# Kernel tuning notes

Hardware: AMD Instinct MI355X
Metric: run time of the kernel (lower is better)

## Reference

```python
import jax, jax.numpy as jnp
import numpy as np

TEMPERATURE = 0.5
IRRELEVANCE_THRESHOLD = 0.4
LN_EPS = 1e-5
NORM_EPS = 1e-12


def setup_inputs() -> dict:
    key = jax.random.key(0)
    ks = jax.random.split(key, 8)
    B, T, D = 32, 4096, 256  # D = 4 * config.embed_dim
    H = D // 2  # relevance encoder output dim = 128
    x = jax.random.normal(ks[0], (B, T, D), dtype=jnp.float32)
    W1 = jax.random.normal(ks[1], (D, D), dtype=jnp.float32) * (1.0 / np.sqrt(D))
    b1 = jnp.zeros((D,), dtype=jnp.float32)
    ln_g = jnp.ones((D,), dtype=jnp.float32)
    ln_b = jnp.zeros((D,), dtype=jnp.float32)
    W2 = jax.random.normal(ks[2], (D, H), dtype=jnp.float32) * (1.0 / np.sqrt(D))
    b2 = jnp.zeros((H,), dtype=jnp.float32)
    topic_query = jax.random.normal(ks[3], (1, 1, D), dtype=jnp.float32)
    spectral_filter = jnp.ones((4,), dtype=jnp.float32) * 0.5
    return {"x": x, "W1": W1, "b1": b1, "ln_g": ln_g, "ln_b": ln_b,
            "W2": W2, "b2": b2, "topic_query": topic_query,
            "spectral_filter": spectral_filter}


def _encode(h, W1, b1, ln_g, ln_b, W2, b2):
    # Linear -> LayerNorm -> GELU(exact) -> Linear
    h = h @ W1 + b1
    mu = jnp.mean(h, axis=-1, keepdims=True)
    var = jnp.mean((h - mu) ** 2, axis=-1, keepdims=True)
    h = (h - mu) / jnp.sqrt(var + LN_EPS) * ln_g + ln_b
    h = jax.nn.gelu(h, approximate=False)
    return h @ W2 + b2


def _l2norm(v):
    n = jnp.sqrt(jnp.sum(v * v, axis=-1, keepdims=True))
    return v / jnp.maximum(n, NORM_EPS)


def reference(x, W1, b1, ln_g, ln_b, W2, b2, topic_query, spectral_filter):
    B, T, D = x.shape
    # --- extract main topic: learned-query attention over time ---
    q = jnp.broadcast_to(topic_query, (B, 1, D))
    scores = jnp.einsum('bqd,btd->bqt', q, x) / TEMPERATURE  # [B,1,T]
    weights = jax.nn.softmax(scores, axis=-1)
    main_topic = jnp.einsum('bqt,btd->bqd', weights, x)  # [B,1,D]
    # --- relevance scores: cosine sim in encoded space ---
    x_enc = _encode(x, W1, b1, ln_g, ln_b, W2, b2)            # [B,T,D/2]
    t_enc = _encode(main_topic, W1, b1, ln_g, ln_b, W2, b2)   # [B,1,D/2]
    relevance = jnp.sum(_l2norm(x_enc) * _l2norm(t_enc), axis=-1)  # [B,T]
    # --- masked complex spectral filtering on quaternion view ---
    irrelevant = relevance < IRRELEVANCE_THRESHOLD  # [B,T]
    x_quat = x.reshape(B, T, D // 4, 4)
    x_fft = jnp.fft.fft(x_quat, axis=1)  # complex64 [B,T,D/4,4]
    filt = jnp.exp(1j * spectral_filter.astype(jnp.complex64))  # [4]
    x_fft = jnp.where(irrelevant[:, :, None, None], x_fft * filt, x_fft)
    x_filtered = jnp.fft.ifft(x_fft, axis=1).real
    return x_filtered.reshape(B, T, D)
```

## Files before the change

kernel.cpp:

```cpp
#include <hip/hip_runtime.h>
#include <math.h>

typedef float f32x4 __attribute__((ext_vector_type(4)));
typedef __bf16 bh8 __attribute__((ext_vector_type(8)));

constexpr int Bc = 32;
constexpr int Tc = 4096;
constexpr int Dc = 256;
constexpr int Hc = 128;
constexpr float kTempInv = 2.0f;
constexpr float kThr = 0.4f;
constexpr float kLnEps = 1e-5f;
constexpr float kNormEps = 1e-12f;
constexpr float kInvSqrt2 = 0.70710678118654752440f;

__device__ __forceinline__ unsigned short f2bf(float f) {
  unsigned u = __float_as_uint(f);
  u += 0x7FFFu + ((u >> 16) & 1u);
  return (unsigned short)(u >> 16);
}
__device__ __forceinline__ float bf2f(unsigned short s) {
  return __uint_as_float(((unsigned)s) << 16);
}

__global__ __launch_bounds__(256) void k_scores(const float* __restrict__ x,
                                                const float* __restrict__ tq,
                                                float* __restrict__ scores) {
  const int wave = threadIdx.x >> 6;
  const int lane = threadIdx.x & 63;
  const int base = blockIdx.x * 32 + wave * 8;
  const float4 q4 = reinterpret_cast<const float4*>(tq)[lane];
  for (int i = 0; i < 8; ++i) {
    const int tok = base + i;
    const float4 xv = reinterpret_cast<const float4*>(x + (size_t)tok * Dc)[lane];
    float p = xv.x * q4.x + xv.y * q4.y + xv.z * q4.z + xv.w * q4.w;
    #pragma unroll
    for (int off = 32; off > 0; off >>= 1) p += __shfl_xor(p, off, 64);
    if (lane == 0) scores[tok] = p * kTempInv;
  }
}

__global__ __launch_bounds__(1024) void k_smstats(const float* __restrict__ scores,
                                                  float2* __restrict__ stats) {
  const int b = blockIdx.x, tid = threadIdx.x;
  const float4 v = reinterpret_cast<const float4*>(scores + (size_t)b * Tc)[tid];
  __shared__ float red[16];
  float m = fmaxf(fmaxf(v.x, v.y), fmaxf(v.z, v.w));
  #pragma unroll
  for (int off = 32; off > 0; off >>= 1) m = fmaxf(m, __shfl_xor(m, off, 64));
  if ((tid & 63) == 0) red[tid >> 6] = m;
  __syncthreads();
  if (tid == 0) {
    float gm = red[0];
    for (int i = 1; i < 16; ++i) gm = fmaxf(gm, red[i]);
    red[0] = gm;
  }
  __syncthreads();
  const float gmax = red[0];
  float s = expf(v.x - gmax) + expf(v.y - gmax) + expf(v.z - gmax) + expf(v.w - gmax);
  #pragma unroll
  for (int off = 32; off > 0; off >>= 1) s += __shfl_xor(s, off, 64);
  __syncthreads();
  if ((tid & 63) == 0) red[tid >> 6] = s;
  __syncthreads();
  if (tid == 0) {
    float t = 0.0f;
    for (int i = 0; i < 16; ++i) t += red[i];
    stats[b] = make_float2(gmax, t);
  }
}

__global__ __launch_bounds__(256) void k_wsum(const float* __restrict__ x,
                                              const float* __restrict__ scores,
                                              const float2* __restrict__ stats,
                                              float* __restrict__ mt) {
  const int b = blockIdx.x >> 4;
  const int chunk = blockIdx.x & 15;
  const int d = threadIdx.x;
  const float2 st = stats[b];
  const int t0 = chunk * 256;
  const float* xb = x + ((size_t)b * Tc + t0) * Dc + d;
  const float* sb = scores + (size_t)b * Tc + t0;
  float acc = 0.0f;
  for (int i = 0; i < 256; ++i) {
    const float w = expf(sb[i] - st.x);
    acc += w * xb[(size_t)i * Dc];
  }
  atomicAdd(&mt[b * Dc + d], acc * (1.0f / st.y));
}

__global__ __launch_bounds__(256) void k_tenc(
    const float* __restrict__ mt, const float* __restrict__ W1,
    const float* __restrict__ b1, const float* __restrict__ lng,
    const float* __restrict__ lnb, const float* __restrict__ W2,
    const float* __restrict__ b2, float* __restrict__ tnorm) {
  const int b = blockIdx.x, j = threadIdx.x;
  __shared__ float v[Dc];
  __shared__ float g[Dc];
  __shared__ float red[4];
  v[j] = mt[b * Dc + j];
  __syncthreads();
  float h = b1[j];
  for (int k = 0; k < Dc; ++k) h += v[k] * W1[(size_t)k * Dc + j];
  float s = h;
  #pragma unroll
  for (int off = 32; off > 0; off >>= 1) s += __shfl_xor(s, off, 64);
  if ((j & 63) == 0) red[j >> 6] = s;
  __syncthreads();
  const float mu = (red[0] + red[1] + red[2] + red[3]) * (1.0f / Dc);
  __syncthreads();
  const float dev = h - mu;
  float q = dev * dev;
  #pragma unroll
  for (int off = 32; off > 0; off >>= 1) q += __shfl_xor(q, off, 64);
  if ((j & 63) == 0) red[j >> 6] = q;
  __syncthreads();
  const float var = (red[0] + red[1] + red[2] + red[3]) * (1.0f / Dc);
  float hn = dev / sqrtf(var + kLnEps) * lng[j] + lnb[j];
  hn = 0.5f * hn * (1.0f + erff(hn * kInvSqrt2));
  g[j] = hn;
  __syncthreads();
  float z = 0.0f;
  if (j < Hc) {
    z = b2[j];
    for (int k = 0; k < Dc; ++k) z += g[k] * W2[(size_t)k * Hc + j];
  }
  float q2 = z * z;
  #pragma unroll
  for (int off = 32; off > 0; off >>= 1) q2 += __shfl_xor(q2, off, 64);
  __syncthreads();
  if ((j & 63) == 0) red[j >> 6] = q2;
  __syncthreads();
  if (j < Hc) {
    const float nrm = sqrtf(red[0] + red[1] + red[2] + red[3]);
    tnorm[b * Hc + j] = z / fmaxf(nrm, kNormEps);
  }
}

__global__ __launch_bounds__(256) void k_prep(const float* __restrict__ W1,
                                              const float* __restrict__ W2,
                                              unsigned short* __restrict__ w1h,
                                              unsigned short* __restrict__ w1l,
                                              unsigned short* __restrict__ w2h,
                                              unsigned short* __restrict__ w2l) {
  const int g = blockIdx.x * 256 + threadIdx.x;
  if (blockIdx.x < 64) {
    const int n = g >> 6;
    const int kq = (g & 63) * 4;
    unsigned h[2] = {0, 0}, l[2] = {0, 0};
    #pragma unroll
    for (int j = 0; j < 4; ++j) {
      const float v = W1[(size_t)(kq + j) * Dc + n];
      const unsigned short hb = f2bf(v);
      const unsigned short lb = f2bf(v - bf2f(hb));
      h[j >> 1] |= ((unsigned)hb) << ((j & 1) * 16);
      l[j >> 1] |= ((unsigned)lb) << ((j & 1) * 16);
    }
    *reinterpret_cast<uint2*>(&w1h[(size_t)n * Dc + kq]) = make_uint2(h[0], h[1]);
    *reinterpret_cast<uint2*>(&w1l[(size_t)n * Dc + kq]) = make_uint2(l[0], l[1]);
  } else {
    const int g2 = g - 16384;
    const int n = g2 >> 6;
    const int kq = (g2 & 63) * 4;
    unsigned h[2] = {0, 0}, l[2] = {0, 0};
    #pragma unroll
    for (int j = 0; j < 4; ++j) {
      const float v = W2[(size_t)(kq + j) * Hc + n];
      const unsigned short hb = f2bf(v);
      const unsigned short lb = f2bf(v - bf2f(hb));
      h[j >> 1] |= ((unsigned)hb) << ((j & 1) * 16);
      l[j >> 1] |= ((unsigned)lb) << ((j & 1) * 16);
    }
    *reinterpret_cast<uint2*>(&w2h[(size_t)n * Dc + kq]) = make_uint2(h[0], h[1]);
    *reinterpret_cast<uint2*>(&w2l[(size_t)n * Dc + kq]) = make_uint2(l[0], l[1]);
  }
}

__global__ __launch_bounds__(256, 2) void k_encode_mfma(
    const float* __restrict__ x,
    const unsigned short* __restrict__ w1h, const unsigned short* __restrict__ w1l,
    const unsigned short* __restrict__ w2h, const unsigned short* __restrict__ w2l,
    const float* __restrict__ b1, const float* __restrict__ lng,
    const float* __restrict__ lnb, const float* __restrict__ b2,
    const float* __restrict__ tnorm, unsigned char* __restrict__ irr) {
  constexpr int LDB = 264;
  constexpr int LDH = 260;
  __shared__ __align__(16) char uni[64 * LDB * 2 * 2];
  __shared__ float ps[2][64];
  __shared__ float psD[2][64];
  __shared__ float p_b1[Dc], p_g[Dc], p_bb[Dc], p_b2[Hc], p_tn[Hc];
  unsigned short* xh_hi = reinterpret_cast<unsigned short*>(uni);
  unsigned short* xh_lo = xh_hi + 64 * LDB;
  float* hbuf = reinterpret_cast<float*>(uni);

  const int tid = threadIdx.x;
  const size_t tok0 = (size_t)blockIdx.x * 64;
  const int b = (int)(tok0 >> 12);
  const int lane = tid & 63;
  const int wave = tid >> 6;
  const int wm = wave >> 1, wn = wave & 1;
  const int lrow = lane & 15, lkh = lane >> 4;

  p_b1[tid] = b1[tid];
  p_g[tid] = lng[tid];
  p_bb[tid] = lnb[tid];
  if (tid < Hc) {
    p_b2[tid] = b2[tid];
    p_tn[tid] = tnorm[b * Hc + tid];
  }
  #pragma unroll
  for (int i = 0; i < 16; ++i) {
    const int f = tid + (i << 8);
    const int row = f >> 6, c4 = f & 63;
    const float4 v = reinterpret_cast<const float4*>(x + (tok0 + row) * Dc)[c4];
    unsigned hp[2] = {0, 0}, lp[2] = {0, 0};
    const float vv[4] = {v.x, v.y, v.z, v.w};
    #pragma unroll
    for (int j = 0; j < 4; ++j) {
      const unsigned short hb = f2bf(vv[j]);
      const unsigned short lb = f2bf(vv[j] - bf2f(hb));
      hp[j >> 1] |= ((unsigned)hb) << ((j & 1) * 16);
      lp[j >> 1] |= ((unsigned)lb) << ((j & 1) * 16);
    }
    *reinterpret_cast<uint2*>(&xh_hi[row * LDB + c4 * 4]) = make_uint2(hp[0], hp[1]);
    *reinterpret_cast<uint2*>(&xh_lo[row * LDB + c4 * 4]) = make_uint2(lp[0], lp[1]);
  }
  __syncthreads();

  f32x4 acc1[2][8];
  #pragma unroll
  for (int mt = 0; mt < 2; ++mt)
    #pragma unroll
    for (int nt = 0; nt < 8; ++nt) acc1[mt][nt] = (f32x4){0.f, 0.f, 0.f, 0.f};

  for (int ks = 0; ks < 8; ++ks) {
    bh8 ah[2], al[2];
    #pragma unroll
    for (int mt = 0; mt < 2; ++mt) {
      const int off = (wm * 32 + mt * 16 + lrow) * LDB + ks * 32 + lkh * 8;
      ah[mt] = *reinterpret_cast<const bh8*>(&xh_hi[off]);
      al[mt] = *reinterpret_cast<const bh8*>(&xh_lo[off]);
    }
    #pragma unroll
    for (int nt = 0; nt < 8; ++nt) {
      const size_t boff = (size_t)(wn * 128 + nt * 16 + lrow) * Dc + ks * 32 + lkh * 8;
      const bh8 bh = *reinterpret_cast<const bh8*>(&w1h[boff]);
      const bh8 bl = *reinterpret_cast<const bh8*>(&w1l[boff]);
      #pragma unroll
      for (int mt = 0; mt < 2; ++mt) {
        acc1[mt][nt] = __builtin_amdgcn_mfma_f32_16x16x32_bf16(ah[mt], bh, acc1[mt][nt], 0, 0, 0);
        acc1[mt][nt] = __builtin_amdgcn_mfma_f32_16x16x32_bf16(al[mt], bh, acc1[mt][nt], 0, 0, 0);
        acc1[mt][nt] = __builtin_amdgcn_mfma_f32_16x16x32_bf16(ah[mt], bl, acc1[mt][nt], 0, 0, 0);
      }
    }
  }
  __syncthreads();

  float s[2][4];
  #pragma unroll
  for (int mt = 0; mt < 2; ++mt)
    #pragma unroll
    for (int j = 0; j < 4; ++j) s[mt][j] = 0.0f;
  #pragma unroll
  for (int nt = 0; nt < 8; ++nt) {
    const int col = wn * 128 + nt * 16 + lrow;
    const float bv = p_b1[col];
    #pragma unroll
    for (int mt = 0; mt < 2; ++mt) {
      #pragma unroll
      for (int j = 0; j < 4; ++j) {
        acc1[mt][nt][j] += bv;
        s[mt][j] += acc1[mt][nt][j];
      }
    }
  }
  #pragma unroll
  for (int mt = 0; mt < 2; ++mt)
    #pragma unroll
    for (int j = 0; j < 4; ++j) {
      #pragma unroll
      for (int off = 8; off > 0; off >>= 1) s[mt][j] += __shfl_xor(s[mt][j], off, 64);
    }
  if (lrow == 0) {
    #pragma unroll
    for (int mt = 0; mt < 2; ++mt)
      #pragma unroll
      for (int j = 0; j < 4; ++j)
        ps[wn][wm * 32 + mt * 16 + lkh * 4 + j] = s[mt][j];
  }
  __syncthreads();
  float mu[2][4];
  #pragma unroll
  for (int mt = 0; mt < 2; ++mt)
    #pragma unroll
    for (int j = 0; j < 4; ++j) {
      const int r = wm * 32 + mt * 16 + lkh * 4 + j;
      mu[mt][j] = (ps[0][r] + ps[1][r]) * (1.0f / Dc);
    }
  float q[2][4];
  #pragma unroll
  for (int mt = 0; mt < 2; ++mt)
    #pragma unroll
    for (int j = 0; j < 4; ++j) q[mt][j] = 0.0f;
  #pragma unroll
  for (int nt = 0; nt < 8; ++nt)
    #pragma unroll
    for (int mt = 0; mt < 2; ++mt)
      #pragma unroll
      for (int j = 0; j < 4; ++j) {
        const float d = acc1[mt][nt][j] - mu[mt][j];
        q[mt][j] += d * d;
      }
  #pragma unroll
  for (int mt = 0; mt < 2; ++mt)
    #pragma unroll
    for (int j = 0; j < 4; ++j) {
      #pragma unroll
      for (int off = 8; off > 0; off >>= 1) q[mt][j] += __shfl_xor(q[mt][j], off, 64);
    }
  if (lrow == 0) {
    #pragma unroll
    for (int mt = 0; mt < 2; ++mt)
      #pragma unroll
      for (int j = 0; j < 4; ++j)
        psD[wn][wm * 32 + mt * 16 + lkh * 4 + j] = q[mt][j];
  }
  __syncthreads();
  float inv[2][4];
  #pragma unroll
  for (int mt = 0; mt < 2; ++mt)
    #pragma unroll
    for (int j = 0; j < 4; ++j) {
      const int r = wm * 32 + mt * 16 + lkh * 4 + j;
      const float var = (psD[0][r] + psD[1][r]) * (1.0f / Dc);
      inv[mt][j] = 1.0f / sqrtf(var + kLnEps);
    }
  #pragma unroll
  for (int nt = 0; nt < 8; ++nt) {
    const int col = wn * 128 + nt * 16 + lrow;
    const float gv = p_g[col], bb = p_bb[col];
    #pragma unroll
    for (int mt = 0; mt < 2; ++mt)
      #pragma unroll
      for (int j = 0; j < 4; ++j) {
        float hv = (acc1[mt][nt][j] - mu[mt][j]) * inv[mt][j] * gv + bb;
        hv = 0.5f * hv * (1.0f + erff(hv * kInvSqrt2));
        hbuf[(wm * 32 + mt * 16 + lkh * 4 + j) * LDH + col] = hv;
      }
  }
  __syncthreads();

  f32x4 acc2[2][4];
  #pragma unroll
  for (int mt = 0; mt < 2; ++mt)
    #pragma unroll
    for (int nt = 0; nt < 4; ++nt) acc2[mt][nt] = (f32x4){0.f, 0.f, 0.f, 0.f};

  for (int ks = 0; ks < 8; ++ks) {
    bh8 ah[2], al[2];
    #pragma unroll
    for (int mt = 0; mt < 2; ++mt) {
      const int base = (wm * 32 + mt * 16 + lrow) * LDH + ks * 32 + lkh * 8;
      const f32x4 u0 = *reinterpret_cast<const f32x4*>(&hbuf[base]);
      const f32x4 u1 = *reinterpret_cast<const f32x4*>(&hbuf[base + 4]);
      union { unsigned short us[8]; bh8 v; } uh, ul;
      #pragma unroll
      for (int j = 0; j < 4; ++j) {
        const unsigned short hb = f2bf(u0[j]);
        uh.us[j] = hb;
        ul.us[j] = f2bf(u0[j] - bf2f(hb));
      }
      #pragma unroll
      for (int j = 0; j < 4; ++j) {
        const unsigned short hb = f2bf(u1[j]);
        uh.us[4 + j] = hb;
        ul.us[4 + j] = f2bf(u1[j] - bf2f(hb));
      }
      ah[mt] = uh.v;
      al[mt] = ul.v;
    }
    #pragma unroll
    for (int nt = 0; nt < 4; ++nt) {
      const size_t boff = (size_t)(wn * 64 + nt * 16 + lrow) * Dc + ks * 32 + lkh * 8;
      const bh8 bh = *reinterpret_cast<const bh8*>(&w2h[boff]);
      const bh8 bl = *reinterpret_cast<const bh8*>(&w2l[boff]);
      #pragma unroll
      for (int mt = 0; mt < 2; ++mt) {
        acc2[mt][nt] = __builtin_amdgcn_mfma_f32_16x16x32_bf16(ah[mt], bh, acc2[mt][nt], 0, 0, 0);
        acc2[mt][nt] = __builtin_amdgcn_mfma_f32_16x16x32_bf16(al[mt], bh, acc2[mt][nt], 0, 0, 0);
        acc2[mt][nt] = __builtin_amdgcn_mfma_f32_16x16x32_bf16(ah[mt], bl, acc2[mt][nt], 0, 0, 0);
      }
    }
  }

  float ss[2][4], sd[2][4];
  #pragma unroll
  for (int mt = 0; mt < 2; ++mt)
    #pragma unroll
    for (int j = 0; j < 4; ++j) { ss[mt][j] = 0.0f; sd[mt][j] = 0.0f; }
  #pragma unroll
  for (int nt = 0; nt < 4; ++nt) {
    const int col2 = wn * 64 + nt * 16 + lrow;
    const float b2v = p_b2[col2], tv = p_tn[col2];
    #pragma unroll
    for (int mt = 0; mt < 2; ++mt)
      #pragma unroll
      for (int j = 0; j < 4; ++j) {
        const float z = acc2[mt][nt][j] + b2v;
        ss[mt][j] += z * z;
        sd[mt][j] += z * tv;
      }
  }
  #pragma unroll
  for (int mt = 0; mt < 2; ++mt)
    #pragma unroll
    for (int j = 0; j < 4; ++j) {
      #pragma unroll
      for (int off = 8; off > 0; off >>= 1) {
        ss[mt][j] += __shfl_xor(ss[mt][j], off, 64);
        sd[mt][j] += __shfl_xor(sd[mt][j], off, 64);
      }
    }
  if (lrow == 0) {
    #pragma unroll
    for (int mt = 0; mt < 2; ++mt)
      #pragma unroll
      for (int j = 0; j < 4; ++j) {
        const int r = wm * 32 + mt * 16 + lkh * 4 + j;
        ps[wn][r] = ss[mt][j];
        psD[wn][r] = sd[mt][j];
      }
  }
  __syncthreads();
  if (tid < 64) {
    const float S = ps[0][tid] + ps[1][tid];
    const float Dd = psD[0][tid] + psD[1][tid];
    const float rel = Dd / fmaxf(sqrtf(S), kNormEps);
    irr[tok0 + tid] = (rel < kThr) ? (unsigned char)1 : (unsigned char)0;
  }
}

__global__ __launch_bounds__(256) void k_transpose(const float* __restrict__ in,
                                                   float* __restrict__ out,
                                                   int R, int C) {
  __shared__ float t[64][65];
  const int tilesC = C >> 6;
  const int perB = (R >> 6) * tilesC;
  const int bid = blockIdx.x;
  const int b = bid / perB;
  const int rem = bid % perB;
  const int tr = rem / tilesC, tc = rem % tilesC;
  const float* ib = in + (size_t)b * R * C;
  float* ob = out + (size_t)b * R * C;
  const int c = threadIdx.x & 63;
  const int r0 = threadIdx.x >> 6;
  #pragma unroll
  for (int i = 0; i < 16; ++i) {
    const int r = r0 + i * 4;
    t[r][c] = ib[(size_t)(tr * 64 + r) * C + tc * 64 + c];
  }
  __syncthreads();
  #pragma unroll
  for (int i = 0; i < 16; ++i) {
    const int r = r0 + i * 4;
    ob[(size_t)(tc * 64 + r) * R + tr * 64 + c] = t[c][r];
  }
}

__device__ __forceinline__ void fft_stages(float2* bufA, float2* bufB,
                                           const float2* tw, int tid, float sign) {
  float2* src = bufA;
  float2* dst = bufB;
  int s = 1;
  for (int stage = 0; stage < 12; ++stage) {
    const int notm = ~(s - 1);
    #pragma unroll
    for (int i = 0; i < 8; ++i) {
      const int r = tid + (i << 8);
      const float2 a = src[r];
      const float2 b = src[r + 2048];
      const float2 w = tw[r & notm];
      const float wy = w.y * sign;
      const float dr = a.x - b.x;
      const float di = a.y - b.y;
      const int d0 = r + (r & notm);
      dst[d0] = make_float2(a.x + b.x, a.y + b.y);
      dst[d0 + s] = make_float2(dr * w.x - di * wy, dr * wy + di * w.x);
    }
    __syncthreads();
    float2* t = src; src = dst; dst = t;
    s <<= 1;
  }
}

__device__ __forceinline__ void mask_pair(float2* buf, const unsigned char* __restrict__ irb,
                                          int k, float ca, float sa, float cb, float sb) {
  const int m = (4096 - k) & 4095;
  const bool ik = irb[k] != 0;
  const bool im = irb[m] != 0;
  const float2 Zk = buf[k];
  const float2 Zm = buf[m];
  const float Ar = 0.5f * (Zk.x + Zm.x), Ai = 0.5f * (Zk.y - Zm.y);
  const float Br = 0.5f * (Zk.y + Zm.y), Bi = -0.5f * (Zk.x - Zm.x);
  const float Gar = 0.5f * ((ik ? ca : 1.0f) + (im ? ca : 1.0f));
  const float Gai = 0.5f * ((ik ? sa : 0.0f) - (im ? sa : 0.0f));
  const float Gbr = 0.5f * ((ik ? cb : 1.0f) + (im ? cb : 1.0f));
  const float Gbi = 0.5f * ((ik ? sb : 0.0f) - (im ? sb : 0.0f));
  const float har = Gar * Ar - Gai * Ai, hai = Gar * Ai + Gai * Ar;
  const float hbr = Gbr * Br - Gbi * Bi, hbi = Gbr * Bi + Gbi * Br;
  buf[k] = make_float2(har - hbi, hai + hbr);
  buf[m] = make_float2(har + hbi, hbr - hai);
}

__global__ __launch_bounds__(256) void k_fft_filter(const float* __restrict__ x,
                                                    const unsigned char* __restrict__ irr,
                                                    const float* __restrict__ sf,
                                                    float* __restrict__ out) {
  __shared__ float2 bufA[4096];
  __shared__ float2 bufB[4096];
  __shared__ float2 tw[2048];
  const int b = blockIdx.x >> 7;
  const int pr = blockIdx.x & 127;
  const int c0 = pr * 2;
  const int tid = threadIdx.x;
  for (int i = tid; i < 2048; i += 256) {
    float sn, cn;
    sincosf(-1.5339807878856412e-3f * (float)i, &sn, &cn);
    tw[i] = make_float2(cn, sn);
  }
  const float* xb = x + ((size_t)b * Tc) * Dc + c0;
  #pragma unroll
  for (int i = 0; i < 16; ++i) {
    const int t = tid + (i << 8);
    bufA[t] = *reinterpret_cast<const float2*>(xb + (size_t)t * Dc);
  }
  __syncthreads();
  fft_stages(bufA, bufB, tw, tid, 1.0f);
  float sa, ca, sb, cb;
  sincosf(sf[c0 & 3], &sa, &ca);
  sincosf(sf[(c0 + 1) & 3], &sb, &cb);
  const unsigned char* irb = irr + (size_t)b * Tc;
  #pragma unroll
  for (int i = 0; i < 8; ++i) mask_pair(bufA, irb, tid + (i << 8), ca, sa, cb, sb);
  if (tid == 0) mask_pair(bufA, irb, 2048, ca, sa, cb, sb);
  __syncthreads();
  fft_stages(bufA, bufB, tw, tid, -1.0f);
  float* ob = out + ((size_t)b * Tc) * Dc + c0;
  constexpr float invN = 1.0f / 4096.0f;
  #pragma unroll
  for (int i = 0; i < 16; ++i) {
    const int t = tid + (i << 8);
    const float2 y = bufA[t];
    *reinterpret_cast<float2*>(ob + (size_t)t * Dc) = make_float2(y.x * invN, y.y * invN);
  }
}

__global__ __launch_bounds__(256) void k_fft_filterT(float* __restrict__ xT,
                                                     const unsigned char* __restrict__ irr,
                                                     const float* __restrict__ sf) {
  __shared__ float2 bufA[4096];
  __shared__ float2 bufB[4096];
  __shared__ float2 tw[2048];
  const int b = blockIdx.x >> 7;
  const int pr = blockIdx.x & 127;
  const int c0 = pr * 2;
  const int tid = threadIdx.x;
  for (int i = tid; i < 2048; i += 256) {
    float sn, cn;
    sincosf(-1.5339807878856412e-3f * (float)i, &sn, &cn);
    tw[i] = make_float2(cn, sn);
  }
  float* r0 = xT + (size_t)(b * Dc + c0) * Tc;
  float* r1 = r0 + Tc;
  #pragma unroll
  for (int i = 0; i < 4; ++i) {
    const int idx = tid + (i << 8);
    const float4 a0 = reinterpret_cast<const float4*>(r0)[idx];
    const float4 a1 = reinterpret_cast<const float4*>(r1)[idx];
    const int t4 = idx * 4;
    bufA[t4 + 0] = make_float2(a0.x, a1.x);
    bufA[t4 + 1] = make_float2(a0.y, a1.y);
    bufA[t4 + 2] = make_float2(a0.z, a1.z);
    bufA[t4 + 3] = make_float2(a0.w, a1.w);
  }
  __syncthreads();
  fft_stages(bufA, bufB, tw, tid, 1.0f);
  float sa, ca, sb, cb;
  sincosf(sf[c0 & 3], &sa, &ca);
  sincosf(sf[(c0 + 1) & 3], &sb, &cb);
  const unsigned char* irb = irr + (size_t)b * Tc;
  #pragma unroll
  for (int i = 0; i < 8; ++i) mask_pair(bufA, irb, tid + (i << 8), ca, sa, cb, sb);
  if (tid == 0) mask_pair(bufA, irb, 2048, ca, sa, cb, sb);
  __syncthreads();
  fft_stages(bufA, bufB, tw, tid, -1.0f);
  constexpr float invN = 1.0f / 4096.0f;
  #pragma unroll
  for (int i = 0; i < 4; ++i) {
    const int idx = tid + (i << 8);
    const int t4 = idx * 4;
    const float2 y0 = bufA[t4 + 0], y1 = bufA[t4 + 1];
    const float2 y2 = bufA[t4 + 2], y3 = bufA[t4 + 3];
    reinterpret_cast<float4*>(r0)[idx] =
        make_float4(y0.x * invN, y1.x * invN, y2.x * invN, y3.x * invN);
    reinterpret_cast<float4*>(r1)[idx] =
        make_float4(y0.y * invN, y1.y * invN, y2.y * invN, y3.y * invN);
  }
}

extern "C" void kernel_launch(void* const* d_in, const int* in_sizes, int n_in,
                              void* d_out, int out_size, void* d_ws, size_t ws_size,
                              hipStream_t stream) {
  const float* x   = (const float*)d_in[0];
  const float* W1  = (const float*)d_in[1];
  const float* b1  = (const float*)d_in[2];
  const float* lng = (const float*)d_in[3];
  const float* lnb = (const float*)d_in[4];
  const float* W2  = (const float*)d_in[5];
  const float* b2  = (const float*)d_in[6];
  const float* tq  = (const float*)d_in[7];
  const float* sf  = (const float*)d_in[8];
  float* out = (float*)d_out;

  char* ws = (char*)d_ws;
  float* scores        = (float*)(ws);
  unsigned short* w1h  = (unsigned short*)(ws);
  unsigned short* w1l  = (unsigned short*)(ws + 131072);
  unsigned short* w2h  = (unsigned short*)(ws + 262144);
  unsigned short* w2l  = (unsigned short*)(ws + 327680);
  float* mt            = (float*)(ws + 524288);
  float2* stats        = (float2*)(ws + 557056);
  float* tnorm         = (float*)(ws + 557312);
  unsigned char* irr   = (unsigned char*)(ws + 573696);
  float* xT            = (float*)(ws + 2097152);
  const bool bigws = ws_size >= (size_t)2097152 + (size_t)134217728;

  hipMemsetAsync(mt, 0, Bc * Dc * sizeof(float), stream);

  k_scores<<<Bc * Tc / 32, 256, 0, stream>>>(x, tq, scores);
  k_smstats<<<Bc, 1024, 0, stream>>>(scores, stats);
  k_wsum<<<Bc * 16, 256, 0, stream>>>(x, scores, stats, mt);
  k_prep<<<96, 256, 0, stream>>>(W1, W2, w1h, w1l, w2h, w2l);
  k_tenc<<<Bc, 256, 0, stream>>>(mt, W1, b1, lng, lnb, W2, b2, tnorm);
  if (bigws) {
    k_transpose<<<Bc * 64 * 4, 256, 0, stream>>>(x, xT, Tc, Dc);
  }
  k_encode_mfma<<<Bc * Tc / 64, 256, 0, stream>>>(x, w1h, w1l, w2h, w2l,
                                                  b1, lng, lnb, b2, tnorm, irr);
  if (bigws) {
    k_fft_filterT<<<Bc * (Dc / 2), 256, 0, stream>>>(xT, irr, sf);
    k_transpose<<<Bc * 4 * 64, 256, 0, stream>>>(xT, out, Dc, Tc);
  } else {
    k_fft_filter<<<Bc * (Dc / 2), 256, 0, stream>>>(x, irr, sf, out);
  }
}
```

Before: 779.5 us.

## Replace transpose+radix-2 FFT with fused radix-4 FFT and shrink encoder LDS

```diff
diff --git a/kernel.cpp b/kernel.cpp
--- a/kernel.cpp
+++ b/kernel.cpp
@@ -176,22 +176,19 @@
   }
 }
 
-__global__ __launch_bounds__(256, 2) void k_encode_mfma(
+__global__ __launch_bounds__(256, 4) void k_encode_mfma(
     const float* __restrict__ x,
     const unsigned short* __restrict__ w1h, const unsigned short* __restrict__ w1l,
     const unsigned short* __restrict__ w2h, const unsigned short* __restrict__ w2l,
     const float* __restrict__ b1, const float* __restrict__ lng,
     const float* __restrict__ lnb, const float* __restrict__ b2,
     const float* __restrict__ tnorm, unsigned char* __restrict__ irr) {
-  constexpr int LDB = 264;
-  constexpr int LDH = 260;
-  __shared__ __align__(16) char uni[64 * LDB * 2 * 2];
+  constexpr int LH = 136;
+  __shared__ __align__(16) unsigned short s_hi[64 * LH];
+  __shared__ __align__(16) unsigned short s_lo[64 * LH];
   __shared__ float ps[2][64];
   __shared__ float psD[2][64];
   __shared__ float p_b1[Dc], p_g[Dc], p_bb[Dc], p_b2[Hc], p_tn[Hc];
-  unsigned short* xh_hi = reinterpret_cast<unsigned short*>(uni);
-  unsigned short* xh_lo = xh_hi + 64 * LDB;
-  float* hbuf = reinterpret_cast<float*>(uni);
 
   const int tid = threadIdx.x;
   const size_t tok0 = (size_t)blockIdx.x * 64;
@@ -208,24 +205,6 @@
     p_b2[tid] = b2[tid];
     p_tn[tid] = tnorm[b * Hc + tid];
   }
-  #pragma unroll
-  for (int i = 0; i < 16; ++i) {
-    const int f = tid + (i << 8);
-    const int row = f >> 6, c4 = f & 63;
-    const float4 v = reinterpret_cast<const float4*>(x + (tok0 + row) * Dc)[c4];
-    unsigned hp[2] = {0, 0}, lp[2] = {0, 0};
-    const float vv[4] = {v.x, v.y, v.z, v.w};
-    #pragma unroll
-    for (int j = 0; j < 4; ++j) {
-      const unsigned short hb = f2bf(vv[j]);
-      const unsigned short lb = f2bf(vv[j] - bf2f(hb));
-      hp[j >> 1] |= ((unsigned)hb) << ((j & 1) * 16);
-      lp[j >> 1] |= ((unsigned)lb) << ((j & 1) * 16);
-    }
-    *reinterpret_cast<uint2*>(&xh_hi[row * LDB + c4 * 4]) = make_uint2(hp[0], hp[1]);
-    *reinterpret_cast<uint2*>(&xh_lo[row * LDB + c4 * 4]) = make_uint2(lp[0], lp[1]);
-  }
-  __syncthreads();
 
   f32x4 acc1[2][8];
   #pragma unroll
@@ -233,28 +212,59 @@
     #pragma unroll
     for (int nt = 0; nt < 8; ++nt) acc1[mt][nt] = (f32x4){0.f, 0.f, 0.f, 0.f};
 
-  for (int ks = 0; ks < 8; ++ks) {
-    bh8 ah[2], al[2];
-    #pragma unroll
-    for (int mt = 0; mt < 2; ++mt) {
-      const int off = (wm * 32 + mt * 16 + lrow) * LDB + ks * 32 + lkh * 8;
-      ah[mt] = *reinterpret_cast<const bh8*>(&xh_hi[off]);
-      al[mt] = *reinterpret_cast<const bh8*>(&xh_lo[off]);
-    }
-    #pragma unroll
-    for (int nt = 0; nt < 8; ++nt) {
-      const size_t boff = (size_t)(wn * 128 + nt * 16 + lrow) * Dc + ks * 32 + lkh * 8;
-      const bh8 bh = *reinterpret_cast<const bh8*>(&w1h[boff]);
-      const bh8 bl = *reinterpret_cast<const bh8*>(&w1l[boff]);
+  auto stage_half = [&](int kh) {
+    #pragma unroll
+    for (int i = 0; i < 8; ++i) {
+      const int f = tid + (i << 8);
+      const int row = f >> 5, c4 = f & 31;
+      const float4 v = *reinterpret_cast<const float4*>(
+          x + (tok0 + row) * Dc + kh * 128 + c4 * 4);
+      unsigned hp[2] = {0, 0}, lp[2] = {0, 0};
+      const float vv[4] = {v.x, v.y, v.z, v.w};
+      #pragma unroll
+      for (int j = 0; j < 4; ++j) {
+        const unsigned short hb = f2bf(vv[j]);
+        const unsigned short lb = f2bf(vv[j] - bf2f(hb));
+        hp[j >> 1] |= ((unsigned)hb) << ((j & 1) * 16);
+        lp[j >> 1] |= ((unsigned)lb) << ((j & 1) * 16);
+      }
+      *reinterpret_cast<uint2*>(&s_hi[row * LH + c4 * 4]) = make_uint2(hp[0], hp[1]);
+      *reinterpret_cast<uint2*>(&s_lo[row * LH + c4 * 4]) = make_uint2(lp[0], lp[1]);
+    }
+  };
+
+  auto gemm1_half = [&](int kh) {
+    for (int ks = 0; ks < 4; ++ks) {
+      bh8 ah[2], al[2];
       #pragma unroll
       for (int mt = 0; mt < 2; ++mt) {
-        acc1[mt][nt] = __builtin_amdgcn_mfma_f32_16x16x32_bf16(ah[mt], bh, acc1[mt][nt], 0, 0, 0);
-        acc1[mt][nt] = __builtin_amdgcn_mfma_f32_16x16x32_bf16(al[mt], bh, acc1[mt][nt], 0, 0, 0);
-        acc1[mt][nt] = __builtin_amdgcn_mfma_f32_16x16x32_bf16(ah[mt], bl, acc1[mt][nt], 0, 0, 0);
-      }
-    }
-  }
-  __syncthreads();
+        const int off = (wm * 32 + mt * 16 + lrow) * LH + ks * 32 + lkh * 8;
+        ah[mt] = *reinterpret_cast<const bh8*>(&s_hi[off]);
+        al[mt] = *reinterpret_cast<const bh8*>(&s_lo[off]);
+      }
+      #pragma unroll
+      for (int nt = 0; nt < 8; ++nt) {
+        const size_t boff = (size_t)(wn * 128 + nt * 16 + lrow) * Dc +
+                            kh * 128 + ks * 32 + lkh * 8;
+        const bh8 bh = *reinterpret_cast<const bh8*>(&w1h[boff]);
+        const bh8 bl = *reinterpret_cast<const bh8*>(&w1l[boff]);
+        #pragma unroll
+        for (int mt = 0; mt < 2; ++mt) {
+          acc1[mt][nt] = __builtin_amdgcn_mfma_f32_16x16x32_bf16(ah[mt], bh, acc1[mt][nt], 0, 0, 0);
+          acc1[mt][nt] = __builtin_amdgcn_mfma_f32_16x16x32_bf16(al[mt], bh, acc1[mt][nt], 0, 0, 0);
+          acc1[mt][nt] = __builtin_amdgcn_mfma_f32_16x16x32_bf16(ah[mt], bl, acc1[mt][nt], 0, 0, 0);
+        }
+      }
+    }
+  };
+
+  stage_half(0);
+  __syncthreads();
+  gemm1_half(0);
+  __syncthreads();
+  stage_half(1);
+  __syncthreads();
+  gemm1_half(1);
 
   float s[2][4];
   #pragma unroll
@@ -326,29 +336,21 @@
         psD[wn][wm * 32 + mt * 16 + lkh * 4 + j] = q[mt][j];
   }
   __syncthreads();
-  float inv[2][4];
   #pragma unroll
   for (int mt = 0; mt < 2; ++mt)
     #pragma unroll
     for (int j = 0; j < 4; ++j) {
       const int r = wm * 32 + mt * 16 + lkh * 4 + j;
       const float var = (psD[0][r] + psD[1][r]) * (1.0f / Dc);
-      inv[mt][j] = 1.0f / sqrtf(var + kLnEps);
-    }
-  #pragma unroll
-  for (int nt = 0; nt < 8; ++nt) {
-    const int col = wn * 128 + nt * 16 + lrow;
-    const float gv = p_g[col], bb = p_bb[col];
-    #pragma unroll
-    for (int mt = 0; mt < 2; ++mt)
-      #pragma unroll
-      for (int j = 0; j < 4; ++j) {
-        float hv = (acc1[mt][nt][j] - mu[mt][j]) * inv[mt][j] * gv + bb;
+      const float inv = 1.0f / sqrtf(var + kLnEps);
+      #pragma unroll
+      for (int nt = 0; nt < 8; ++nt) {
+        const int col = wn * 128 + nt * 16 + lrow;
+        float hv = (acc1[mt][nt][j] - mu[mt][j]) * inv * p_g[col] + p_bb[col];
         hv = 0.5f * hv * (1.0f + erff(hv * kInvSqrt2));
-        hbuf[(wm * 32 + mt * 16 + lkh * 4 + j) * LDH + col] = hv;
-      }
-  }
-  __syncthreads();
+        acc1[mt][nt][j] = hv;
+      }
+    }
 
   f32x4 acc2[2][4];
   #pragma unroll
@@ -356,42 +358,56 @@
     #pragma unroll
     for (int nt = 0; nt < 4; ++nt) acc2[mt][nt] = (f32x4){0.f, 0.f, 0.f, 0.f};
 
-  for (int ks = 0; ks < 8; ++ks) {
-    bh8 ah[2], al[2];
-    #pragma unroll
-    for (int mt = 0; mt < 2; ++mt) {
-      const int base = (wm * 32 + mt * 16 + lrow) * LDH + ks * 32 + lkh * 8;
-      const f32x4 u0 = *reinterpret_cast<const f32x4*>(&hbuf[base]);
-      const f32x4 u1 = *reinterpret_cast<const f32x4*>(&hbuf[base + 4]);
-      union { unsigned short us[8]; bh8 v; } uh, ul;
-      #pragma unroll
-      for (int j = 0; j < 4; ++j) {
-        const unsigned short hb = f2bf(u0[j]);
-        uh.us[j] = hb;
-        ul.us[j] = f2bf(u0[j] - bf2f(hb));
-      }
-      #pragma unroll
-      for (int j = 0; j < 4; ++j) {
-        const unsigned short hb = f2bf(u1[j]);
-        uh.us[4 + j] = hb;
-        ul.us[4 + j] = f2bf(u1[j] - bf2f(hb));
-      }
-      ah[mt] = uh.v;
-      al[mt] = ul.v;
-    }
-    #pragma unroll
-    for (int nt = 0; nt < 4; ++nt) {
-      const size_t boff = (size_t)(wn * 64 + nt * 16 + lrow) * Dc + ks * 32 + lkh * 8;
-      const bh8 bh = *reinterpret_cast<const bh8*>(&w2h[boff]);
-      const bh8 bl = *reinterpret_cast<const bh8*>(&w2l[boff]);
+  auto hwrite = [&](int half) {
+    if (wn == half) {
+      #pragma unroll
+      for (int nt = 0; nt < 8; ++nt) {
+        const int colg = nt * 16 + lrow;
+        #pragma unroll
+        for (int mt = 0; mt < 2; ++mt)
+          #pragma unroll
+          for (int j = 0; j < 4; ++j) {
+            const int row = wm * 32 + mt * 16 + lkh * 4 + j;
+            const float hv = acc1[mt][nt][j];
+            const unsigned short hb = f2bf(hv);
+            s_hi[row * LH + colg] = hb;
+            s_lo[row * LH + colg] = f2bf(hv - bf2f(hb));
+          }
+      }
+    }
+  };
+  auto gemm2_half = [&](int kh) {
+    for (int ks = 0; ks < 4; ++ks) {
+      bh8 ah[2], al[2];
       #pragma unroll
       for (int mt = 0; mt < 2; ++mt) {
-        acc2[mt][nt] = __builtin_amdgcn_mfma_f32_16x16x32_bf16(ah[mt], bh, acc2[mt][nt], 0, 0, 0);
-        acc2[mt][nt] = __builtin_amdgcn_mfma_f32_16x16x32_bf16(al[mt], bh, acc2[mt][nt], 0, 0, 0);
-        acc2[mt][nt] = __builtin_amdgcn_mfma_f32_16x16x32_bf16(ah[mt], bl, acc2[mt][nt], 0, 0, 0);
-      }
-    }
-  }
+        const int off = (wm * 32 + mt * 16 + lrow) * LH + ks * 32 + lkh * 8;
+        ah[mt] = *reinterpret_cast<const bh8*>(&s_hi[off]);
+        al[mt] = *reinterpret_cast<const bh8*>(&s_lo[off]);
+      }
+      #pragma unroll
+      for (int nt = 0; nt < 4; ++nt) {
+        const size_t boff = (size_t)(wn * 64 + nt * 16 + lrow) * Dc +
+                            kh * 128 + ks * 32 + lkh * 8;
+        const bh8 bh = *reinterpret_cast<const bh8*>(&w2h[boff]);
+        const bh8 bl = *reinterpret_cast<const bh8*>(&w2l[boff]);
+        #pragma unroll
+        for (int mt = 0; mt < 2; ++mt) {
+          acc2[mt][nt] = __builtin_amdgcn_mfma_f32_16x16x32_bf16(ah[mt], bh, acc2[mt][nt], 0, 0, 0);
+          acc2[mt][nt] = __builtin_amdgcn_mfma_f32_16x16x32_bf16(al[mt], bh, acc2[mt][nt], 0, 0, 0);
+          acc2[mt][nt] = __builtin_amdgcn_mfma_f32_16x16x32_bf16(ah[mt], bl, acc2[mt][nt], 0, 0, 0);
+        }
+      }
+    }
+  };
+
+  hwrite(0);
+  __syncthreads();
+  gemm2_half(0);
+  __syncthreads();
+  hwrite(1);
+  __syncthreads();
+  gemm2_half(1);
 
   float ss[2][4], sd[2][4];
   #pragma unroll
@@ -440,56 +456,44 @@
   }
 }
 
-__global__ __launch_bounds__(256) void k_transpose(const float* __restrict__ in,
-                                                   float* __restrict__ out,
-                                                   int R, int C) {
-  __shared__ float t[64][65];
-  const int tilesC = C >> 6;
-  const int perB = (R >> 6) * tilesC;
-  const int bid = blockIdx.x;
-  const int b = bid / perB;
-  const int rem = bid % perB;
-  const int tr = rem / tilesC, tc = rem % tilesC;
-  const float* ib = in + (size_t)b * R * C;
-  float* ob = out + (size_t)b * R * C;
-  const int c = threadIdx.x & 63;
-  const int r0 = threadIdx.x >> 6;
-  #pragma unroll
-  for (int i = 0; i < 16; ++i) {
-    const int r = r0 + i * 4;
-    t[r][c] = ib[(size_t)(tr * 64 + r) * C + tc * 64 + c];
-  }
-  __syncthreads();
-  #pragma unroll
-  for (int i = 0; i < 16; ++i) {
-    const int r = r0 + i * 4;
-    ob[(size_t)(tc * 64 + r) * R + tr * 64 + c] = t[c][r];
-  }
-}
-
-__device__ __forceinline__ void fft_stages(float2* bufA, float2* bufB,
-                                           const float2* tw, int tid, float sign) {
-  float2* src = bufA;
-  float2* dst = bufB;
-  int s = 1;
-  for (int stage = 0; stage < 12; ++stage) {
-    const int notm = ~(s - 1);
-    #pragma unroll
-    for (int i = 0; i < 8; ++i) {
-      const int r = tid + (i << 8);
-      const float2 a = src[r];
-      const float2 b = src[r + 2048];
-      const float2 w = tw[r & notm];
-      const float wy = w.y * sign;
-      const float dr = a.x - b.x;
-      const float di = a.y - b.y;
-      const int d0 = r + (r & notm);
-      dst[d0] = make_float2(a.x + b.x, a.y + b.y);
-      dst[d0 + s] = make_float2(dr * w.x - di * wy, dr * wy + di * w.x);
+__device__ __forceinline__ float2 cmul(const float2 w, const float2 v) {
+  return make_float2(w.x * v.x - w.y * v.y, w.x * v.y + w.y * v.x);
+}
+
+__device__ void fft4_run(float2* A0, float2* B0, float2* A1, float2* B1,
+                         const float2* __restrict__ tw, const int tid,
+                         const float sgn) {
+  float2 *s0 = A0, *d0 = B0, *s1 = A1, *d1 = B1;
+  int sdiv = 1;
+  for (int st = 0; st < 6; ++st) {
+    const int qq = tid & (sdiv - 1);
+    const int ti = tid - qq;
+    float2 w1 = tw[ti];
+    w1.y *= sgn;
+    const float2 w2 = cmul(w1, w1);
+    const float2 w3 = cmul(w2, w1);
+    const int wb = (ti << 2) + qq;
+    #pragma unroll
+    for (int sq = 0; sq < 2; ++sq) {
+      const float2* S = sq ? s1 : s0;
+      float2* D = sq ? d1 : d0;
+      const float2 a = S[tid];
+      const float2 b = S[tid + 1024];
+      const float2 c = S[tid + 2048];
+      const float2 d = S[tid + 3072];
+      const float apcx = a.x + c.x, apcy = a.y + c.y;
+      const float amcx = a.x - c.x, amcy = a.y - c.y;
+      const float bpdx = b.x + d.x, bpdy = b.y + d.y;
+      const float bmdx = (b.x - d.x) * sgn, bmdy = (b.y - d.y) * sgn;
+      D[wb] = make_float2(apcx + bpdx, apcy + bpdy);
+      D[wb + sdiv] = cmul(w1, make_float2(amcx + bmdy, amcy - bmdx));
+      D[wb + 2 * sdiv] = cmul(w2, make_float2(apcx - bpdx, apcy - bpdy));
+      D[wb + 3 * sdiv] = cmul(w3, make_float2(amcx - bmdy, amcy + bmdx));
     }
     __syncthreads();
-    float2* t = src; src = dst; dst = t;
-    s <<= 1;
+    float2* t = s0; s0 = d0; d0 = t;
+    t = s1; s1 = d1; d1 = t;
+    sdiv <<= 2;
   }
 }
 
@@ -512,99 +516,64 @@
   buf[m] = make_float2(har + hbi, hbr - hai);
 }
 
-__global__ __launch_bounds__(256) void k_fft_filter(const float* __restrict__ x,
-                                                    const unsigned char* __restrict__ irr,
-                                                    const float* __restrict__ sf,
-                                                    float* __restrict__ out) {
-  __shared__ float2 bufA[4096];
-  __shared__ float2 bufB[4096];
-  __shared__ float2 tw[2048];
-  const int b = blockIdx.x >> 7;
-  const int pr = blockIdx.x & 127;
-  const int c0 = pr * 2;
+__global__ __launch_bounds__(1024) void k_fft4(const float* __restrict__ x,
+                                               const unsigned char* __restrict__ irr,
+                                               const float* __restrict__ sf,
+                                               float* __restrict__ out) {
+  __shared__ float2 SA0[4096];
+  __shared__ float2 SB0[4096];
+  __shared__ float2 SA1[4096];
+  __shared__ float2 SB1[4096];
+  __shared__ float2 tw[1024];
+  const int bb = blockIdx.x >> 6;
+  const int g = blockIdx.x & 63;
   const int tid = threadIdx.x;
-  for (int i = tid; i < 2048; i += 256) {
+  {
     float sn, cn;
-    sincosf(-1.5339807878856412e-3f * (float)i, &sn, &cn);
-    tw[i] = make_float2(cn, sn);
-  }
-  const float* xb = x + ((size_t)b * Tc) * Dc + c0;
-  #pragma unroll
-  for (int i = 0; i < 16; ++i) {
-    const int t = tid + (i << 8);
-    bufA[t] = *reinterpret_cast<const float2*>(xb + (size_t)t * Dc);
-  }
-  __syncthreads();
-  fft_stages(bufA, bufB, tw, tid, 1.0f);
-  float sa, ca, sb, cb;
-  sincosf(sf[c0 & 3], &sa, &ca);
-  sincosf(sf[(c0 + 1) & 3], &sb, &cb);
-  const unsigned char* irb = irr + (size_t)b * Tc;
-  #pragma unroll
-  for (int i = 0; i < 8; ++i) mask_pair(bufA, irb, tid + (i << 8), ca, sa, cb, sb);
-  if (tid == 0) mask_pair(bufA, irb, 2048, ca, sa, cb, sb);
-  __syncthreads();
-  fft_stages(bufA, bufB, tw, tid, -1.0f);
-  float* ob = out + ((size_t)b * Tc) * Dc + c0;
+    sincosf(-1.5339807878856412e-3f * (float)tid, &sn, &cn);
+    tw[tid] = make_float2(cn, sn);
+  }
+  const float4* xb = reinterpret_cast<const float4*>(x + (size_t)bb * Tc * Dc) + g;
+  #pragma unroll
+  for (int j = 0; j < 4; ++j) {
+    const int t = tid + (j << 10);
+    const float4 v = xb[(size_t)t * 64];
+    SA0[t] = make_float2(v.x, v.y);
+    SA1[t] = make_float2(v.z, v.w);
+  }
+  __syncthreads();
+
+  fft4_run(SA0, SB0, SA1, SB1, tw, tid, 1.0f);
+
+  float ca0, sa0, cb0, sb0, ca1, sa1, cb1, sb1;
+  sincosf(sf[0], &sa0, &ca0);
+  sincosf(sf[1], &sb0, &cb0);
+  sincosf(sf[2], &sa1, &ca1);
+  sincosf(sf[3], &sb1, &cb1);
+  const unsigned char* irb = irr + (size_t)bb * Tc;
+  #pragma unroll
+  for (int i = 0; i < 2; ++i) {
+    const int k = tid + (i << 10);
+    mask_pair(SA0, irb, k, ca0, sa0, cb0, sb0);
+    mask_pair(SA1, irb, k, ca1, sa1, cb1, sb1);
+  }
+  if (tid == 0) {
+    mask_pair(SA0, irb, 2048, ca0, sa0, cb0, sb0);
+    mask_pair(SA1, irb, 2048, ca1, sa1, cb1, sb1);
+  }
+  __syncthreads();
+
+  fft4_run(SA0, SB0, SA1, SB1, tw, tid, -1.0f);
+
+  float4* ob = reinterpret_cast<float4*>(out + (size_t)bb * Tc * Dc) + g;
   constexpr float invN = 1.0f / 4096.0f;
   #pragma unroll
-  for (int i = 0; i < 16; ++i) {
-    const int t = tid + (i << 8);
-    const float2 y = bufA[t];
-    *reinterpret_cast<float2*>(ob + (size_t)t * Dc) = make_float2(y.x * invN, y.y * invN);
-  }
-}
-
-__global__ __launch_bounds__(256) void k_fft_filterT(float* __restrict__ xT,
-                                                     const unsigned char* __restrict__ irr,
-                                                     const float* __restrict__ sf) {
-  __shared__ float2 bufA[4096];
-  __shared__ float2 bufB[4096];
-  __shared__ float2 tw[2048];
-  const int b = blockIdx.x >> 7;
-  const int pr = blockIdx.x & 127;
-  const int c0 = pr * 2;
-  const int tid = threadIdx.x;
-  for (int i = tid; i < 2048; i += 256) {
-    float sn, cn;
-    sincosf(-1.5339807878856412e-3f * (float)i, &sn, &cn);
-    tw[i] = make_float2(cn, sn);
-  }
-  float* r0 = xT + (size_t)(b * Dc + c0) * Tc;
-  float* r1 = r0 + Tc;
-  #pragma unroll
-  for (int i = 0; i < 4; ++i) {
-    const int idx = tid + (i << 8);
-    const float4 a0 = reinterpret_cast<const float4*>(r0)[idx];
-    const float4 a1 = reinterpret_cast<const float4*>(r1)[idx];
-    const int t4 = idx * 4;
-    bufA[t4 + 0] = make_float2(a0.x, a1.x);
-    bufA[t4 + 1] = make_float2(a0.y, a1.y);
-    bufA[t4 + 2] = make_float2(a0.z, a1.z);
-    bufA[t4 + 3] = make_float2(a0.w, a1.w);
-  }
-  __syncthreads();
-  fft_stages(bufA, bufB, tw, tid, 1.0f);
-  float sa, ca, sb, cb;
-  sincosf(sf[c0 & 3], &sa, &ca);
-  sincosf(sf[(c0 + 1) & 3], &sb, &cb);
-  const unsigned char* irb = irr + (size_t)b * Tc;
-  #pragma unroll
-  for (int i = 0; i < 8; ++i) mask_pair(bufA, irb, tid + (i << 8), ca, sa, cb, sb);
-  if (tid == 0) mask_pair(bufA, irb, 2048, ca, sa, cb, sb);
-  __syncthreads();
-  fft_stages(bufA, bufB, tw, tid, -1.0f);
-  constexpr float invN = 1.0f / 4096.0f;
-  #pragma unroll
-  for (int i = 0; i < 4; ++i) {
-    const int idx = tid + (i << 8);
-    const int t4 = idx * 4;
-    const float2 y0 = bufA[t4 + 0], y1 = bufA[t4 + 1];
-    const float2 y2 = bufA[t4 + 2], y3 = bufA[t4 + 3];
-    reinterpret_cast<float4*>(r0)[idx] =
-        make_float4(y0.x * invN, y1.x * invN, y2.x * invN, y3.x * invN);
-    reinterpret_cast<float4*>(r1)[idx] =
-        make_float4(y0.y * invN, y1.y * invN, y2.y * invN, y3.y * invN);
+  for (int j = 0; j < 4; ++j) {
+    const int t = tid + (j << 10);
+    const float2 y0 = SA0[t];
+    const float2 y1 = SA1[t];
+    ob[(size_t)t * 64] = make_float4(y0.x * invN, y0.y * invN,
+                                     y1.x * invN, y1.y * invN);
   }
 }
 
@@ -632,8 +601,6 @@
   float2* stats        = (float2*)(ws + 557056);
   float* tnorm         = (float*)(ws + 557312);
   unsigned char* irr   = (unsigned char*)(ws + 573696);
-  float* xT            = (float*)(ws + 2097152);
-  const bool bigws = ws_size >= (size_t)2097152 + (size_t)134217728;
 
   hipMemsetAsync(mt, 0, Bc * Dc * sizeof(float), stream);
 
@@ -642,15 +609,7 @@
   k_wsum<<<Bc * 16, 256, 0, stream>>>(x, scores, stats, mt);
   k_prep<<<96, 256, 0, stream>>>(W1, W2, w1h, w1l, w2h, w2l);
   k_tenc<<<Bc, 256, 0, stream>>>(mt, W1, b1, lng, lnb, W2, b2, tnorm);
-  if (bigws) {
-    k_transpose<<<Bc * 64 * 4, 256, 0, stream>>>(x, xT, Tc, Dc);
-  }
   k_encode_mfma<<<Bc * Tc / 64, 256, 0, stream>>>(x, w1h, w1l, w2h, w2l,
                                                   b1, lng, lnb, b2, tnorm, irr);
-  if (bigws) {
-    k_fft_filterT<<<Bc * (Dc / 2), 256, 0, stream>>>(xT, irr, sf);
-    k_transpose<<<Bc * 4 * 64, 256, 0, stream>>>(xT, out, Dc, Tc);
-  } else {
-    k_fft_filter<<<Bc * (Dc / 2), 256, 0, stream>>>(x, irr, sf, out);
-  }
-}
+  k_fft4<<<Bc * 64, 1024, 0, stream>>>(x, irr, sf, out);
+}
```

Measured after the change: 890.2 us. 1.14x slower.
